# Kernel tuning notes

Measured on AMD Instinct MI355X. Metric: run time of the kernel, lower is better.

## Reference

```python
import jax, jax.numpy as jnp
import numpy as np

B, S, C, H = 2, 512, 25, 768


def setup_inputs() -> dict:
    key = jax.random.key(0)
    ks = jax.random.split(key, 10)
    sc = 1.0 / np.sqrt(H)
    return {
        "token_rep": jax.random.normal(ks[0], (B, S, H), jnp.float32),
        "label_rep": jax.random.normal(ks[1], (B, C, H), jnp.float32),
        # proj_token: Linear(H, 2H) stored as [in, out] for x @ W
        "Wt": jax.random.normal(ks[2], (H, 2 * H), jnp.float32) * sc,
        "bt": jnp.zeros((2 * H,), jnp.float32),
        # proj_label: Linear(H, 2H)
        "Wl": jax.random.normal(ks[3], (H, 2 * H), jnp.float32) * sc,
        "bl": jnp.zeros((2 * H,), jnp.float32),
        # out_mlp[0]: Linear(3H, 4H)
        "W1": jax.random.normal(ks[4], (3 * H, 4 * H), jnp.float32) * (1.0 / np.sqrt(3 * H)),
        "b1": jnp.zeros((4 * H,), jnp.float32),
        # out_mlp[3]: Linear(4H, 3)
        "W2": jax.random.normal(ks[5], (4 * H, 3), jnp.float32) * (1.0 / np.sqrt(4 * H)),
        "b2": jnp.zeros((3,), jnp.float32),
    }


def reference(token_rep, label_rep, Wt, bt, Wl, bl, W1, b1, W2, b2):
    h = token_rep.shape[-1]
    # project and split into (additive half, multiplicative half)
    tp = token_rep @ Wt + bt            # [B,S,2H]
    lp = label_rep @ Wl + bl            # [B,C,2H]
    ta, tb = tp[..., :h], tp[..., h:]
    la, lb = lp[..., :h], lp[..., h:]
    # First MLP layer on concat([ta, la, tb*lb]) without materializing the concat:
    # split W1 row-wise into the three input blocks.
    W1t, W1l, W1p = W1[:h], W1[h:2 * h], W1[2 * h:]
    hid = (ta @ W1t)[:, :, None, :] \
        + (la @ W1l)[:, None, :, :] \
        + jnp.einsum('bsh,bch,hf->bscf', tb, lb, W1p) \
        + b1                            # [B,S,C,4H]
    # Dropout is identity in eval mode.
    return jax.nn.relu(hid) @ W2 + b2   # [B,S,C,3]
```

## Files before the change

kernel.cpp:

```cpp
#include <hip/hip_runtime.h>
#include <hip/hip_bf16.h>
#include <cstdint>
#include <cstddef>

#define BB 2
#define SS 512
#define CC 25
#define HH 768
#define H2 1536
#define H3 2304
#define H4 3072
#define XC_STRIDE ((size_t)96 * 512 * 8)

typedef __attribute__((ext_vector_type(8))) short bf16x8;
typedef __attribute__((ext_vector_type(4))) float f32x4;

#define DEVINL static __device__ __forceinline__

DEVINL unsigned short f2bf(float f) {
  union { float f; unsigned u; } v; v.f = f;
  unsigned r = v.u + 0x7FFF + ((v.u >> 16) & 1);
  return (unsigned short)(r >> 16);
}
DEVINL float bf2f(unsigned short b) {
  union { unsigned u; float f; } v; v.u = ((unsigned)b) << 16; return v.f;
}

DEVINL void async16(const void* g, void* l) {
  __builtin_amdgcn_global_load_lds(
      (const __attribute__((address_space(1))) void*)g,
      (__attribute__((address_space(3))) void*)l, 16, 0, 0);
}

__global__ void k_prep(const float* __restrict__ token,
                       const float* __restrict__ label,
                       const float* __restrict__ b2,
                       const float* __restrict__ Wt,
                       const float* __restrict__ Wl,
                       const float* __restrict__ W1,
                       unsigned short* __restrict__ TC,
                       unsigned short* __restrict__ LC,
                       float* __restrict__ out,
                       unsigned short* __restrict__ WtC,
                       unsigned short* __restrict__ WlC,
                       unsigned short* __restrict__ W1C) {
  __shared__ float tile[64][33];
  const int bid = blockIdx.x;
  const int tid = threadIdx.x;
  if (bid < 408) {
    const float* in;
    unsigned short* o;
    int R, RP, kt, rt;
    if (bid < 384) {
      in = token; o = TC; R = 1024; RP = 1024; kt = bid % 24; rt = bid / 24;
    } else {
      in = label; o = LC; R = 50; RP = 64; kt = bid - 384; rt = 0;
    }
    const int k0 = kt * 32, r0 = rt * 64;
    const int tx = tid & 31, ty = tid >> 5;
#pragma unroll
    for (int i = 0; i < 8; i++) {
      int r = r0 + ty + i * 8;
      tile[ty + i * 8][tx] = in[(size_t)min(r, R - 1) * HH + k0 + tx];
    }
    __syncthreads();
    const int rl = tid & 63, kcl = tid >> 6;
    bf16x8 ov;
#pragma unroll
    for (int j = 0; j < 8; j++) ov[j] = (short)f2bf(tile[rl][kcl * 8 + j]);
    *(bf16x8*)&o[((size_t)((k0 >> 3) + kcl) * RP + r0 + rl) * 8] = ov;
  } else if (bid < 708) {
    int i = (bid - 408) * 256 + tid;
    if (i < BB * SS * CC * 3) out[i] = b2[i % 3];
  } else {
    const int wb = bid - 708;
    const float* in;
    unsigned short* o;
    int N, bx, by;
    if (wb < 3456) {
      in = W1; o = W1C; N = H4; bx = wb % 48; by = wb / 48;
    } else if (wb < 4032) {
      int b = wb - 3456; in = Wt; o = WtC; N = H2; bx = b % 24; by = b / 24;
    } else {
      int b = wb - 4032; in = Wl; o = WlC; N = H2; bx = b % 24; by = b / 24;
    }
    const int f = bx * 64 + (tid & 63);
    const int hc = by * 4 + (tid >> 6);
    bf16x8 ov;
#pragma unroll
    for (int j = 0; j < 8; j++)
      ov[j] = (short)f2bf(in[(size_t)(hc * 8 + j) * N + f]);
    *(bf16x8*)&o[((size_t)hc * N + f) * 8] = ov;
  }
}

DEVINL void mm_kloop(const unsigned short* __restrict__ Ab, int NRA, int MA,
                     int m0, const unsigned short* __restrict__ Bt, int NRB,
                     int n0, unsigned short* As, unsigned short* Bs,
                     f32x4 (&acc)[4][4]) {
  const int tid = threadIdx.x;
  const int lane = tid & 63;
  const int wave = tid >> 6;
  const int q = lane >> 4;
  const int li = lane & 15;
  const int wm = (wave >> 1) * 64;
  const int wn = (wave & 1) * 64;

  int sr[4], skc[4], sra[4];
#pragma unroll
  for (int j = 0; j < 4; j++) {
    int slot = j * 256 + tid;
    skc[j] = slot >> 7;
    sr[j] = slot & 127;
    sra[j] = min(m0 + sr[j], MA - 1);
  }
  auto stage = [&](int kciter) {
#pragma unroll
    for (int j = 0; j < 4; j++) {
      int slot = j * 256 + tid;
      async16(Ab + ((size_t)(kciter + skc[j]) * NRA + sra[j]) * 8,
              (char*)As + slot * 16);
      async16(Bt + ((size_t)(kciter + skc[j]) * NRB + n0 + sr[j]) * 8,
              (char*)Bs + slot * 16);
    }
  };

  stage(0);
  for (int it = 0; it < 12; it++) {
    __syncthreads();
#pragma unroll
    for (int ks = 0; ks < 2; ks++) {
      bf16x8 af[4], bb[4];
#pragma unroll
      for (int mi = 0; mi < 4; mi++)
        af[mi] = *(const bf16x8*)&As[((ks * 4 + q) * 128 + wm + mi * 16 + li) * 8];
#pragma unroll
      for (int ni = 0; ni < 4; ni++)
        bb[ni] = *(const bf16x8*)&Bs[((ks * 4 + q) * 128 + wn + ni * 16 + li) * 8];
#pragma unroll
      for (int mi = 0; mi < 4; mi++)
#pragma unroll
        for (int ni = 0; ni < 4; ni++)
          acc[mi][ni] = __builtin_amdgcn_mfma_f32_16x16x32_bf16(
              af[mi], bb[ni], acc[mi][ni], 0, 0, 0);
    }
    __syncthreads();
    if (it + 1 < 12) stage((it + 1) * 8);
  }
}

__global__ __launch_bounds__(256, 4) void k_mm1(
    const unsigned short* __restrict__ TC, const unsigned short* __restrict__ LC,
    const unsigned short* __restrict__ WtC, const unsigned short* __restrict__ WlC,
    const float* __restrict__ bt, const float* __restrict__ bl,
    unsigned short* __restrict__ TP, unsigned short* __restrict__ LP) {
  __shared__ __align__(16) unsigned short As[8 * 128 * 8];
  __shared__ __align__(16) unsigned short Bs[8 * 128 * 8];
  const int bid = blockIdx.x;
  const int nt = bid % 12, my = bid / 12;
  const bool tok = my < 8;
  const unsigned short* A = tok ? TC : LC;
  const unsigned short* Bt = tok ? WtC : WlC;
  const float* bias = tok ? bt : bl;
  unsigned short* C = tok ? TP : LP;
  const int NRA = tok ? 1024 : 64, MA = tok ? 1024 : 50;
  const int m0 = tok ? my * 128 : 0;
  const int ldc = NRA;
  const int n0 = nt * 128;

  f32x4 acc[4][4];
#pragma unroll
  for (int i = 0; i < 4; i++)
#pragma unroll
    for (int j = 0; j < 4; j++) acc[i][j] = (f32x4){0.f, 0.f, 0.f, 0.f};
  mm_kloop(A, NRA, MA, m0, Bt, H2, n0, As, Bs, acc);

  const int lane = threadIdx.x & 63, wave = threadIdx.x >> 6;
  const int q = lane >> 4, li = lane & 15;
  const int wm = (wave >> 1) * 64, wn = (wave & 1) * 64;
#pragma unroll
  for (int mi = 0; mi < 4; mi++)
#pragma unroll
    for (int rr = 0; rr < 4; rr++) {
      int row = m0 + wm + mi * 16 + q * 4 + rr;
      if (row < MA) {
#pragma unroll
        for (int ni = 0; ni < 4; ni++) {
          int col = n0 + wn + ni * 16 + li;
          C[((size_t)(col >> 3) * ldc + row) * 8 + (col & 7)] =
              f2bf(acc[mi][ni][rr] + bias[col]);
        }
      }
    }
}

__global__ __launch_bounds__(256, 4) void k_mm2(
    const unsigned short* __restrict__ TP, const unsigned short* __restrict__ LP,
    const unsigned short* __restrict__ W1C,
    float* __restrict__ base, float* __restrict__ al,
    unsigned short* __restrict__ XC) {
  __shared__ __align__(16) unsigned short As[8 * 128 * 8];
  __shared__ __align__(16) unsigned short Bs[8 * 128 * 8];
  const int bid = blockIdx.x;
  if (bid < 216) {
    const int nt = bid % 24, my = bid / 24;
    const bool tok = my < 8;
    const unsigned short* A = tok ? TP : LP;
    const unsigned short* Bt = tok ? W1C : W1C + (size_t)96 * H4 * 8;
    float* Cf = tok ? base : al;
    const int NRA = tok ? 1024 : 64, MA = tok ? 1024 : 50;
    const int m0 = tok ? my * 128 : 0;
    const int n0 = nt * 128;

    f32x4 acc[4][4];
#pragma unroll
    for (int i = 0; i < 4; i++)
#pragma unroll
      for (int j = 0; j < 4; j++) acc[i][j] = (f32x4){0.f, 0.f, 0.f, 0.f};
    mm_kloop(A, NRA, MA, m0, Bt, H4, n0, As, Bs, acc);

    const int lane = threadIdx.x & 63, wave = threadIdx.x >> 6;
    const int q = lane >> 4, li = lane & 15;
    const int wm = (wave >> 1) * 64, wn = (wave & 1) * 64;
#pragma unroll
    for (int mi = 0; mi < 4; mi++)
#pragma unroll
      for (int rr = 0; rr < 4; rr++) {
        int row = m0 + wm + mi * 16 + q * 4 + rr;
        if (row < MA) {
#pragma unroll
          for (int ni = 0; ni < 4; ni++) {
            int col = n0 + wn + ni * 16 + li;
            Cf[(size_t)row * H4 + col] = acc[mi][ni][rr];
          }
        }
      }
  } else {
    const int i = bid - 216;
    const int bc = i / 192;
    const int rem = i % 192;
    const int hc = rem >> 1;
    const int s = (rem & 1) * 256 + threadIdx.x;
    const int b = bc / CC;
    bf16x8 tv = *(const bf16x8*)&TP[((size_t)(96 + hc) * 1024 + b * 512 + s) * 8];
    bf16x8 lv = *(const bf16x8*)&LP[((size_t)(96 + hc) * 64 + bc) * 8];
    bf16x8 o;
#pragma unroll
    for (int j = 0; j < 8; j++)
      o[j] = (short)f2bf(bf2f((unsigned short)tv[j]) * bf2f((unsigned short)lv[j]));
    *(bf16x8*)&XC[(size_t)bc * XC_STRIDE + ((size_t)hc * 512 + s) * 8] = o;
  }
}

__global__ __launch_bounds__(256, 4) void k_scorer(
    const unsigned short* __restrict__ XC,
    const unsigned short* __restrict__ Bt,
    const float* __restrict__ base, const float* __restrict__ al,
    const float* __restrict__ b1, const float* __restrict__ W2,
    float* __restrict__ out) {
  __shared__ __align__(16) unsigned short As[8 * 128 * 8];
  __shared__ __align__(16) unsigned short Bs[8 * 128 * 8];
  const int tid = threadIdx.x;
  const int lane = tid & 63;
  const int wave = tid >> 6;
  const int q = lane >> 4;
  const int li = lane & 15;
  const int wm = (wave >> 1) * 64;
  const int wn = (wave & 1) * 64;

  const int n0 = blockIdx.x * 128;
  const int bc = blockIdx.y >> 2;
  const int m0 = (blockIdx.y & 3) * 128;
  const unsigned short* Ab = XC + (size_t)bc * XC_STRIDE;

  f32x4 acc[4][4];
#pragma unroll
  for (int i = 0; i < 4; i++)
#pragma unroll
    for (int j = 0; j < 4; j++) acc[i][j] = (f32x4){0.f, 0.f, 0.f, 0.f};
  mm_kloop(Ab, 512, 512, m0, Bt, H4, n0, As, Bs, acc);

  const int b = bc / CC, c = bc % CC;
  int fcol[4];
  float alb[4];
#pragma unroll
  for (int ni = 0; ni < 4; ni++) {
    int f = n0 + wn + ni * 16 + li;
    fcol[ni] = f;
    alb[ni] = al[(size_t)bc * H4 + f] + b1[f];
  }
  bf16x8 w2f[2];
#pragma unroll
  for (int ks = 0; ks < 2; ks++)
#pragma unroll
    for (int jj = 0; jj < 8; jj++) {
      int f = n0 + wn + ks * 32 + q * 8 + jj;
      float v = (li < 3) ? W2[(size_t)f * 3 + li] : 0.f;
      w2f[ks][jj] = (short)f2bf(v);
    }
  unsigned short* Ew = (unsigned short*)((char*)As + wave * 2304);

#pragma unroll
  for (int mi = 0; mi < 4; mi++) {
    float bs[4][4];
#pragma unroll
    for (int rr = 0; rr < 4; rr++) {
      int s_l = m0 + wm + mi * 16 + q * 4 + rr;
      const float* bp = base + (size_t)(b * SS + s_l) * H4;
#pragma unroll
      for (int ni = 0; ni < 4; ni++) bs[ni][rr] = bp[fcol[ni]];
    }
#pragma unroll
    for (int rr = 0; rr < 4; rr++)
#pragma unroll
      for (int ni = 0; ni < 4; ni++) {
        float v = acc[mi][ni][rr] + bs[ni][rr] + alb[ni];
        v = fmaxf(v, 0.f);
        Ew[(q * 4 + rr) * 72 + ni * 16 + li] = f2bf(v);
      }
    f32x4 oc = (f32x4){0.f, 0.f, 0.f, 0.f};
#pragma unroll
    for (int ks = 0; ks < 2; ks++) {
      bf16x8 ef = *(const bf16x8*)&Ew[li * 72 + ks * 32 + q * 8];
      oc = __builtin_amdgcn_mfma_f32_16x16x32_bf16(ef, w2f[ks], oc, 0, 0, 0);
    }
#pragma unroll
    for (int rr = 0; rr < 4; rr++) {
      int s_l = m0 + wm + mi * 16 + q * 4 + rr;
      if (li < 3)
        atomicAdd(&out[((size_t)(b * SS + s_l) * CC + c) * 3 + li], oc[rr]);
    }
  }
}


extern "C" void kernel_launch(void* const* d_in, const int* in_sizes, int n_in,
                              void* d_out, int out_size, void* d_ws, size_t ws_size,
                              hipStream_t stream) {
  (void)in_sizes; (void)n_in; (void)ws_size; (void)out_size;
  const float* token = (const float*)d_in[0];
  const float* label = (const float*)d_in[1];
  const float* Wt    = (const float*)d_in[2];
  const float* bt    = (const float*)d_in[3];
  const float* Wl    = (const float*)d_in[4];
  const float* bl    = (const float*)d_in[5];
  const float* W1    = (const float*)d_in[6];
  const float* b1    = (const float*)d_in[7];
  const float* W2    = (const float*)d_in[8];
  const float* b2    = (const float*)d_in[9];
  float* out = (float*)d_out;

  char* p = (char*)d_ws;
  auto alloc = [&](size_t bytes) {
    char* r = p;
    p += (bytes + 255) & ~(size_t)255;
    return r;
  };
  unsigned short* TC  = (unsigned short*)alloc((size_t)96 * 1024 * 8 * 2);
  unsigned short* LC  = (unsigned short*)alloc((size_t)96 * 64 * 8 * 2);
  unsigned short* WtC = (unsigned short*)alloc((size_t)96 * 1536 * 8 * 2);
  unsigned short* WlC = (unsigned short*)alloc((size_t)96 * 1536 * 8 * 2);
  unsigned short* W1C = (unsigned short*)alloc((size_t)288 * 3072 * 8 * 2);
  unsigned short* TP  = (unsigned short*)alloc((size_t)192 * 1024 * 8 * 2);
  unsigned short* LP  = (unsigned short*)alloc((size_t)192 * 64 * 8 * 2);
  unsigned short* XC  = (unsigned short*)alloc((size_t)CC * BB * XC_STRIDE * 2);
  float* base = (float*)alloc((size_t)BB * SS * H4 * 4);
  float* al   = (float*)alloc((size_t)BB * CC * H4 * 4);

  k_prep<<<5316, 256, 0, stream>>>(token, label, b2, Wt, Wl, W1,
                                   TC, LC, out, WtC, WlC, W1C);
  k_mm1<<<108, 256, 0, stream>>>(TC, LC, WtC, WlC, bt, bl, TP, LP);
  k_mm2<<<9816, 256, 0, stream>>>(TP, LP, W1C, base, al, XC);
  k_scorer<<<dim3(24, 200), 256, 0, stream>>>(
      XC, W1C + (size_t)192 * H4 * 8, base, al, b1, W2, out);
}
```

Measured before the change: 270.7 us.

## Enlarge scorer tile to 256x256 with 512 threads and triple-buffered async k-loop

The scorer GEMM moves from 128x128 tiles with 256 threads to 256x256 tiles with 512 threads (8 waves, each computing 128x64). The generic k-loop is replaced by an inline triple-buffered async-copy pipeline with explicit vmcnt waits and MFMA priority bumps. This doubles operand reuse per tile and overlaps global loads with compute. In exchange it raises register pressure (acc grows to 8x4 f32x4), uses more LDS per block, and halves the block count. The epilogue scratch region (Ew) still lives in As, which must be large enough for eight waves.

```diff
diff --git a/kernel.cpp b/kernel.cpp
--- a/kernel.cpp
+++ b/kernel.cpp
@@ -252,33 +252,96 @@
   }
 }
 
-__global__ __launch_bounds__(256, 4) void k_scorer(
+__global__ __launch_bounds__(512, 2) void k_scorer(
     const unsigned short* __restrict__ XC,
     const unsigned short* __restrict__ Bt,
     const float* __restrict__ base, const float* __restrict__ al,
     const float* __restrict__ b1, const float* __restrict__ W2,
     float* __restrict__ out) {
-  __shared__ __align__(16) unsigned short As[8 * 128 * 8];
-  __shared__ __align__(16) unsigned short Bs[8 * 128 * 8];
+  __shared__ __align__(16) unsigned short As[3][4 * 256 * 8];
+  __shared__ __align__(16) unsigned short Bs[3][4 * 256 * 8];
   const int tid = threadIdx.x;
   const int lane = tid & 63;
   const int wave = tid >> 6;
   const int q = lane >> 4;
   const int li = lane & 15;
-  const int wm = (wave >> 1) * 64;
-  const int wn = (wave & 1) * 64;
-
-  const int n0 = blockIdx.x * 128;
-  const int bc = blockIdx.y >> 2;
-  const int m0 = (blockIdx.y & 3) * 128;
+  const int wm = (wave >> 2) * 128;
+  const int wn = (wave & 3) * 64;
+
+  const int n0 = blockIdx.x * 256;
+  const int bc = blockIdx.y >> 1;
+  const int m0 = (blockIdx.y & 1) * 256;
   const unsigned short* Ab = XC + (size_t)bc * XC_STRIDE;
 
-  f32x4 acc[4][4];
-#pragma unroll
-  for (int i = 0; i < 4; i++)
+  int skc[2], srow[2];
+#pragma unroll
+  for (int j = 0; j < 2; j++) {
+    int slot = j * 512 + tid;
+    skc[j] = slot >> 8;
+    srow[j] = slot & 255;
+  }
+  auto stage = [&](int t, int bufsel) {
+    const int kc0 = t * 4;
+#pragma unroll
+    for (int j = 0; j < 2; j++) {
+      int slot = j * 512 + tid;
+      async16(Ab + ((size_t)(kc0 + skc[j]) * 512 + m0 + srow[j]) * 8,
+              (char*)&As[bufsel][0] + slot * 16);
+    }
+#pragma unroll
+    for (int j = 0; j < 2; j++) {
+      int slot = j * 512 + tid;
+      async16(Bt + ((size_t)(kc0 + skc[j]) * 3072 + n0 + srow[j]) * 8,
+              (char*)&Bs[bufsel][0] + slot * 16);
+    }
+  };
+
+  f32x4 acc[8][4];
+#pragma unroll
+  for (int i = 0; i < 8; i++)
 #pragma unroll
     for (int j = 0; j < 4; j++) acc[i][j] = (f32x4){0.f, 0.f, 0.f, 0.f};
-  mm_kloop(Ab, 512, 512, m0, Bt, H4, n0, As, Bs, acc);
+
+  stage(0, 0);
+  stage(1, 1);
+  asm volatile("s_waitcnt vmcnt(4)" ::: "memory");
+  __builtin_amdgcn_s_barrier();
+  asm volatile("" ::: "memory");
+
+  int c0 = 0, c1 = 1, c2 = 2;
+  const int abase = (q * 256 + wm + li) * 8;
+  const int bbase = (q * 256 + wn + li) * 8;
+  for (int v = 0; v < 24; v++) {
+    if (v + 2 < 24) stage(v + 2, c2);
+
+    const unsigned short* Ap = &As[c0][0];
+    const unsigned short* Bp = &Bs[c0][0];
+    bf16x8 af[8], bb[4];
+#pragma unroll
+    for (int mi = 0; mi < 8; mi++)
+      af[mi] = *(const bf16x8*)&Ap[abase + mi * 16 * 8];
+#pragma unroll
+    for (int ni = 0; ni < 4; ni++)
+      bb[ni] = *(const bf16x8*)&Bp[bbase + ni * 16 * 8];
+    __builtin_amdgcn_s_setprio(1);
+#pragma unroll
+    for (int mi = 0; mi < 8; mi++)
+#pragma unroll
+      for (int ni = 0; ni < 4; ni++)
+        acc[mi][ni] = __builtin_amdgcn_mfma_f32_16x16x32_bf16(
+            af[mi], bb[ni], acc[mi][ni], 0, 0, 0);
+    __builtin_amdgcn_s_setprio(0);
+
+    if (v < 23) {
+      if (v < 22)
+        asm volatile("s_waitcnt vmcnt(4) lgkmcnt(0)" ::: "memory");
+      else
+        asm volatile("s_waitcnt vmcnt(0) lgkmcnt(0)" ::: "memory");
+      __builtin_amdgcn_s_barrier();
+      asm volatile("" ::: "memory");
+    }
+    int tmp = c0; c0 = c1; c1 = c2; c2 = tmp;
+  }
 
   const int b = bc / CC, c = bc % CC;
   int fcol[4];
@@ -301,7 +364,7 @@
   unsigned short* Ew = (unsigned short*)((char*)As + wave * 2304);
 
 #pragma unroll
-  for (int mi = 0; mi < 4; mi++) {
+  for (int mi = 0; mi < 8; mi++) {
     float bs[4][4];
 #pragma unroll
     for (int rr = 0; rr < 4; rr++) {
@@ -371,6 +434,6 @@
                                    TC, LC, out, WtC, WlC, W1C);
   k_mm1<<<108, 256, 0, stream>>>(TC, LC, WtC, WlC, bt, bl, TP, LP);
   k_mm2<<<9816, 256, 0, stream>>>(TP, LP, W1C, base, al, XC);
-  k_scorer<<<dim3(24, 200), 256, 0, stream>>>(
+  k_scorer<<<dim3(12, 100), 512, 0, stream>>>(
       XC, W1C + (size_t)192 * H4 * 8, base, al, b1, W2, out);
 }
```

Measured after the change: 334.4 us. 23.5% more time.

## Load scorer A-fragments directly from global into registers, prefetching next k-chunk

Applied to the files above, without the earlier changes.

The scorer GEMM no longer stages the XC activation tile through shared memory. Each wave loads its A fragments straight from global into registers and prefetches the next k-chunk while the current MFMAs run. Only the weight tile B is still copied to LDS asynchronously. This halves LDS use and removes the LDS round trip for A. In exchange it uses more registers (occupancy hint lowered from 4 to 3 blocks), and A is loaded redundantly across waves that share rows.

```diff
diff --git a/kernel.cpp b/kernel.cpp
--- a/kernel.cpp
+++ b/kernel.cpp
@@ -31,6 +31,8 @@
       (const __attribute__((address_space(1))) void*)g,
       (__attribute__((address_space(3))) void*)l, 16, 0, 0);
 }
+
+#define MFMA16(a, b, c) __builtin_amdgcn_mfma_f32_16x16x32_bf16(a, b, c, 0, 0, 0)
 
 __global__ void k_prep(const float* __restrict__ token,
                        const float* __restrict__ label,
@@ -141,8 +143,7 @@
       for (int mi = 0; mi < 4; mi++)
 #pragma unroll
         for (int ni = 0; ni < 4; ni++)
-          acc[mi][ni] = __builtin_amdgcn_mfma_f32_16x16x32_bf16(
-              af[mi], bb[ni], acc[mi][ni], 0, 0, 0);
+          acc[mi][ni] = MFMA16(af[mi], bb[ni], acc[mi][ni]);
     }
     __syncthreads();
     if (it + 1 < 12) stage((it + 1) * 8);
@@ -252,13 +253,21 @@
   }
 }
 
-__global__ __launch_bounds__(256, 4) void k_scorer(
+
+#define STAGE_B4(KC0) do {                                                    \
+    _Pragma("unroll")                                                         \
+    for (int j_ = 0; j_ < 4; j_++) {                                          \
+      int slot_ = j_ * 256 + tid;                                             \
+      async16(Bt + ((size_t)((KC0) + (slot_ >> 7)) * H4 + n0 + (slot_ & 127)) * 8, \
+              (char*)Bs + slot_ * 16);                                        \
+    } } while (0)
+
+__global__ __launch_bounds__(256, 3) void k_scorer(
     const unsigned short* __restrict__ XC,
     const unsigned short* __restrict__ Bt,
     const float* __restrict__ base, const float* __restrict__ al,
     const float* __restrict__ b1, const float* __restrict__ W2,
     float* __restrict__ out) {
-  __shared__ __align__(16) unsigned short As[8 * 128 * 8];
   __shared__ __align__(16) unsigned short Bs[8 * 128 * 8];
   const int tid = threadIdx.x;
   const int lane = tid & 63;
@@ -273,12 +282,61 @@
   const int m0 = (blockIdx.y & 3) * 128;
   const unsigned short* Ab = XC + (size_t)bc * XC_STRIDE;
 
+  const unsigned short* ap[4];
+#pragma unroll
+  for (int mi = 0; mi < 4; mi++)
+    ap[mi] = Ab + (size_t)(m0 + wm + mi * 16 + li) * 8;
+
   f32x4 acc[4][4];
 #pragma unroll
   for (int i = 0; i < 4; i++)
 #pragma unroll
     for (int j = 0; j < 4; j++) acc[i][j] = (f32x4){0.f, 0.f, 0.f, 0.f};
-  mm_kloop(Ab, 512, 512, m0, Bt, H4, n0, As, Bs, acc);
+
+  bf16x8 af0[4], af1[4];
+#pragma unroll
+  for (int mi = 0; mi < 4; mi++)
+    af0[mi] = *(const bf16x8*)(ap[mi] + (size_t)(0 + q) * 4096);
+#pragma unroll
+  for (int mi = 0; mi < 4; mi++)
+    af1[mi] = *(const bf16x8*)(ap[mi] + (size_t)(4 + q) * 4096);
+  STAGE_B4(0);
+
+#pragma unroll 1
+  for (int it = 0; it < 12; it++) {
+    __syncthreads();
+    bf16x8 bb[4];
+#pragma unroll
+    for (int ni = 0; ni < 4; ni++)
+      bb[ni] = *(const bf16x8*)&Bs[((0 + q) * 128 + wn + ni * 16 + li) * 8];
+#pragma unroll
+    for (int mi = 0; mi < 4; mi++)
+#pragma unroll
+      for (int ni = 0; ni < 4; ni++)
+        acc[mi][ni] = MFMA16(af0[mi], bb[ni], acc[mi][ni]);
+    {
+      const int cb0 = (it < 11) ? (it + 1) * 8 : 88;
+#pragma unroll
+      for (int mi = 0; mi < 4; mi++)
+        af0[mi] = *(const bf16x8*)(ap[mi] + (size_t)(cb0 + q) * 4096);
+    }
+#pragma unroll
+    for (int ni = 0; ni < 4; ni++)
+      bb[ni] = *(const bf16x8*)&Bs[((4 + q) * 128 + wn + ni * 16 + li) * 8];
+#pragma unroll
+    for (int mi = 0; mi < 4; mi++)
+#pragma unroll
+      for (int ni = 0; ni < 4; ni++)
+        acc[mi][ni] = MFMA16(af1[mi], bb[ni], acc[mi][ni]);
+    {
+      const int cb1 = (it < 11) ? (it + 1) * 8 + 4 : 92;
+#pragma unroll
+      for (int mi = 0; mi < 4; mi++)
+        af1[mi] = *(const bf16x8*)(ap[mi] + (size_t)(cb1 + q) * 4096);
+    }
+    __syncthreads();
+    if (it < 11) STAGE_B4((it + 1) * 8);
+  }
 
   const int b = bc / CC, c = bc % CC;
   int fcol[4];
@@ -298,7 +356,7 @@
       float v = (li < 3) ? W2[(size_t)f * 3 + li] : 0.f;
       w2f[ks][jj] = (short)f2bf(v);
     }
-  unsigned short* Ew = (unsigned short*)((char*)As + wave * 2304);
+  unsigned short* Ew = (unsigned short*)((char*)Bs + wave * 2304);
 
 #pragma unroll
   for (int mi = 0; mi < 4; mi++) {
@@ -322,7 +380,7 @@
 #pragma unroll
     for (int ks = 0; ks < 2; ks++) {
       bf16x8 ef = *(const bf16x8*)&Ew[li * 72 + ks * 32 + q * 8];
-      oc = __builtin_amdgcn_mfma_f32_16x16x32_bf16(ef, w2f[ks], oc, 0, 0, 0);
+      oc = MFMA16(ef, w2f[ks], oc);
     }
 #pragma unroll
     for (int rr = 0; rr < 4; rr++) {
```

Result: slower. 281.5 us (+4.0%).

## Triple-buffer B in LDS and stream A from global into registers in scorer GEMM

Applied to the files above, without the earlier changes.

The scorer GEMM drops the shared mm_kloop. The B tile is now triple-buffered in LDS with async global-to-LDS loads issued two iterations ahead. The A operand is loaded straight from global memory into registers, double-buffered across iterations, so each k-step needs one barrier, with an explicit vmcnt wait, instead of two. Block indices are also swizzled to group blocks for better L2 reuse, and launch bounds drop to 3 blocks per SM to make room for the extra registers and LDS. The cost is lower occupancy, more register pressure, and hand-counted waitcnt values that must match the number of loads in flight.

```diff
diff --git a/kernel.cpp b/kernel.cpp
--- a/kernel.cpp
+++ b/kernel.cpp
@@ -31,6 +31,11 @@
       (const __attribute__((address_space(1))) void*)g,
       (__attribute__((address_space(3))) void*)l, 16, 0, 0);
 }
+
+#define BAR() do { asm volatile("" ::: "memory"); \
+                   __builtin_amdgcn_s_barrier();  \
+                   asm volatile("" ::: "memory"); } while (0)
+#define MFMA16(a, b, c) __builtin_amdgcn_mfma_f32_16x16x32_bf16(a, b, c, 0, 0, 0)
 
 __global__ void k_prep(const float* __restrict__ token,
                        const float* __restrict__ label,
@@ -141,8 +146,7 @@
       for (int mi = 0; mi < 4; mi++)
 #pragma unroll
         for (int ni = 0; ni < 4; ni++)
-          acc[mi][ni] = __builtin_amdgcn_mfma_f32_16x16x32_bf16(
-              af[mi], bb[ni], acc[mi][ni], 0, 0, 0);
+          acc[mi][ni] = MFMA16(af[mi], bb[ni], acc[mi][ni]);
     }
     __syncthreads();
     if (it + 1 < 12) stage((it + 1) * 8);
@@ -252,14 +256,57 @@
   }
 }
 
-__global__ __launch_bounds__(256, 4) void k_scorer(
+
+#define STAGE_B4(KC0, DST) do {                                               \
+    char* dst_ = (char*)(DST);                                                \
+    _Pragma("unroll")                                                         \
+    for (int j_ = 0; j_ < 4; j_++) {                                          \
+      int slot_ = j_ * 256 + tid;                                             \
+      async16(Bt + ((size_t)((KC0) + (slot_ >> 7)) * H4 + n0 + (slot_ & 127)) * 8, \
+              dst_ + slot_ * 16);                                             \
+    } } while (0)
+
+#define SC_BODY(IT, PREAD, PSTAGE, CA0, CA1, NA0, NA1) do {                   \
+    if ((IT) + 2 < 12) STAGE_B4(((IT) + 2) * 8, (PSTAGE));                    \
+    {                                                                         \
+      const int cbn_ = ((IT) + 1 < 12) ? ((IT) + 1) * 8 : 88;      \
+      _Pragma("unroll")                                                       \
+      for (int mi_ = 0; mi_ < 4; mi_++)                                       \
+        NA0[mi_] = *(const bf16x8*)(ap[mi_] + (size_t)(cbn_ + q) * 4096);     \
+      _Pragma("unroll")                                                       \
+      for (int mi_ = 0; mi_ < 4; mi_++)                                       \
+        NA1[mi_] = *(const bf16x8*)(ap[mi_] + (size_t)(cbn_ + 4 + q) * 4096); \
+    }                                                                         \
+    {                                                                         \
+      bf16x8 bb_[4];                                                          \
+      _Pragma("unroll")                                                       \
+      for (int ni_ = 0; ni_ < 4; ni_++)                                       \
+        bb_[ni_] = *(const bf16x8*)&(PREAD)[((0 + q) * 128 + wn + ni_ * 16 + li) * 8]; \
+      _Pragma("unroll")                                                       \
+      for (int mi_ = 0; mi_ < 4; mi_++)                                       \
+        _Pragma("unroll")                                                     \
+        for (int ni_ = 0; ni_ < 4; ni_++)                                     \
+          acc[mi_][ni_] = MFMA16(CA0[mi_], bb_[ni_], acc[mi_][ni_]);          \
+      _Pragma("unroll")                                                       \
+      for (int ni_ = 0; ni_ < 4; ni_++)                                       \
+        bb_[ni_] = *(const bf16x8*)&(PREAD)[((4 + q) * 128 + wn + ni_ * 16 + li) * 8]; \
+      _Pragma("unroll")                                                       \
+      for (int mi_ = 0; mi_ < 4; mi_++)                                       \
+        _Pragma("unroll")                                                     \
+        for (int ni_ = 0; ni_ < 4; ni_++)                                     \
+          acc[mi_][ni_] = MFMA16(CA1[mi_], bb_[ni_], acc[mi_][ni_]);          \
+    }                                                                         \
+    asm volatile("s_waitcnt vmcnt(16)" ::: "memory");                         \
+    BAR();                                                                    \
+  } while (0)
+
+__global__ __launch_bounds__(256, 3) void k_scorer(
     const unsigned short* __restrict__ XC,
     const unsigned short* __restrict__ Bt,
     const float* __restrict__ base, const float* __restrict__ al,
     const float* __restrict__ b1, const float* __restrict__ W2,
     float* __restrict__ out) {
-  __shared__ __align__(16) unsigned short As[8 * 128 * 8];
-  __shared__ __align__(16) unsigned short Bs[8 * 128 * 8];
+  __shared__ __align__(16) unsigned short Bs[3][8 * 128 * 8];
   const int tid = threadIdx.x;
   const int lane = tid & 63;
   const int wave = tid >> 6;
@@ -268,17 +315,48 @@
   const int wm = (wave >> 1) * 64;
   const int wn = (wave & 1) * 64;
 
-  const int n0 = blockIdx.x * 128;
-  const int bc = blockIdx.y >> 2;
-  const int m0 = (blockIdx.y & 3) * 128;
+  const int lin = blockIdx.y * 24 + blockIdx.x;
+  const int swz = (lin & 7) * 600 + (lin >> 3);
+  const int n0 = (swz % 24) * 128;
+  const int yy = swz / 24;
+  const int bc = yy >> 2;
+  const int m0 = (yy & 3) * 128;
   const unsigned short* Ab = XC + (size_t)bc * XC_STRIDE;
 
+  const unsigned short* ap[4];
+#pragma unroll
+  for (int mi = 0; mi < 4; mi++)
+    ap[mi] = Ab + (size_t)(m0 + wm + mi * 16 + li) * 8;
+
   f32x4 acc[4][4];
 #pragma unroll
   for (int i = 0; i < 4; i++)
 #pragma unroll
     for (int j = 0; j < 4; j++) acc[i][j] = (f32x4){0.f, 0.f, 0.f, 0.f};
-  mm_kloop(Ab, 512, 512, m0, Bt, H4, n0, As, Bs, acc);
+
+  const unsigned short* c0 = &Bs[0][0];
+  const unsigned short* c1 = &Bs[1][0];
+  const unsigned short* c2 = &Bs[2][0];
+
+  bf16x8 a0A[4], a0B[4], a1A[4], a1B[4];
+  STAGE_B4(0, c0);
+  STAGE_B4(8, c1);
+#pragma unroll
+  for (int mi = 0; mi < 4; mi++)
+    a0A[mi] = *(const bf16x8*)(ap[mi] + (size_t)(0 + q) * 4096);
+#pragma unroll
+  for (int mi = 0; mi < 4; mi++)
+    a0B[mi] = *(const bf16x8*)(ap[mi] + (size_t)(4 + q) * 4096);
+  asm volatile("s_waitcnt vmcnt(12)" ::: "memory");
+  BAR();
+
+#pragma unroll 1
+  for (int tt = 0; tt < 6; tt++) {
+    const int itE = 2 * tt;
+    SC_BODY(itE,     c0, c2, a0A, a0B, a1A, a1B);
+    SC_BODY(itE + 1, c1, c0, a1A, a1B, a0A, a0B);
+    const unsigned short* t_ = c2; c2 = c1; c1 = c0; c0 = t_;
+  }
 
   const int b = bc / CC, c = bc % CC;
   int fcol[4];
@@ -298,7 +376,7 @@
       float v = (li < 3) ? W2[(size_t)f * 3 + li] : 0.f;
       w2f[ks][jj] = (short)f2bf(v);
     }
-  unsigned short* Ew = (unsigned short*)((char*)As + wave * 2304);
+  unsigned short* Ew = (unsigned short*)((char*)&Bs[0][0] + wave * 2304);
 
 #pragma unroll
   for (int mi = 0; mi < 4; mi++) {
@@ -322,7 +400,7 @@
 #pragma unroll
     for (int ks = 0; ks < 2; ks++) {
       bf16x8 ef = *(const bf16x8*)&Ew[li * 72 + ks * 32 + q * 8];
-      oc = __builtin_amdgcn_mfma_f32_16x16x32_bf16(ef, w2f[ks], oc, 0, 0, 0);
+      oc = MFMA16(ef, w2f[ks], oc);
     }
 #pragma unroll
     for (int rr = 0; rr < 4; rr++) {
```

New measurement: 295.6 us. 9.2% more time.
